# Kernel tuning notes

Hardware: AMD Instinct MI355X
Metric: run time of the kernel (lower is better)

## Reference

```python
import jax, jax.numpy as jnp
import numpy as np

DIVERSITY_RATE = 0.5


def setup_inputs() -> dict:
    key = jax.random.key(0)
    k1, k2 = jax.random.split(key)
    # model log-probabilities at current step: (bsz, beam, vocab)
    lprobs = jax.nn.log_softmax(
        jax.random.normal(k1, (128, 5, 50257), dtype=jnp.float32), axis=-1
    )
    # historical hypothesis scores: (bsz, beam, step)
    scores = jax.random.normal(k2, (128, 5, 10), dtype=jnp.float32)
    return {"lprobs": lprobs, "scores": scores, "step": 10}


def reference(lprobs, scores, step):
    bsz, beam_size, vocab_size = lprobs.shape
    k = min(beam_size * 2, beam_size * vocab_size - 1)  # = 10 here

    # step > 0 path: accumulate running score of each hypothesis
    lp = lprobs + scores[:, :, step - 1][:, :, None]  # (bsz, beam, vocab)

    # 1/ per-beam top-k over vocab (vectorized over all beams at once)
    s, idx = jax.lax.top_k(lp, k)  # (bsz, beam, k); idx already < vocab (fmod no-op)

    # 2/,3/ intra-sibling ordering -> rank penalty (rank r gets r*rate)
    sibling_score = jnp.arange(1, k + 1, dtype=lp.dtype) * DIVERSITY_RATE  # (k,)
    s = s - sibling_score  # broadcast over (bsz, beam, k)

    # 4/ final top-k over all beam*k candidates
    indices = idx.reshape(bsz, beam_size * k)
    final_scores, flat_pos = jax.lax.top_k(s.reshape(bsz, beam_size * k), k)
    final_beams = flat_pos // k  # which input beam each winner came from
    final_indices = jnp.take_along_axis(indices, flat_pos, axis=1)  # vocab ids

    return final_scores, final_indices, final_beams
```

## Files before the change

kernel.cpp:

```cpp
#include <hip/hip_runtime.h>
#include <hip/hip_bf16.h>
#include <math.h>
#include <stdint.h>


#define BS    256
#define KK    10
#define BEAM  5
#define NSLOT 7
#define CS    (BS * NSLOT * 4)
#define CAP   1024
#define FCAP  2048

typedef unsigned long long u64;

__device__ __forceinline__ uint32_t ford(float x) {
    uint32_t u = __float_as_uint(x);
    return (u & 0x80000000u) ? ~u : (u | 0x80000000u);
}
__device__ __forceinline__ float funord(uint32_t u) {
    return __uint_as_float((u & 0x80000000u) ? (u & 0x7fffffffu) : ~u);
}

__device__ __forceinline__ void insert10(u64 (&key)[KK], u64 k) {
    if (k > key[KK - 1]) {
#pragma unroll
        for (int j = KK - 1; j >= 1; --j)
            key[j] = (k > key[j - 1]) ? key[j - 1] : ((k > key[j]) ? k : key[j]);
        if (k > key[0]) key[0] = k;
    }
}

__global__ __launch_bounds__(BS) void dss_chunk_topk(
    const float* __restrict__ lprobs,
    const float* __restrict__ scores,
    const int*   __restrict__ step_ptr,
    int vocab, int sdim, int nc,
    u64* __restrict__ ws_keys)
{
    const int chunk = blockIdx.x;
    const int row   = blockIdx.y;
    const int tid   = threadIdx.x;
    const int lane  = tid & 63;
    const int step  = step_ptr[0];
    const float bias = scores[(size_t)row * sdim + (step - 1)];

    const int c0 = chunk * CS;
    int len = vocab - c0; if (len > CS) len = CS;
    const float* cp = lprobs + (size_t)row * vocab + c0;

    __shared__ u64   cand[CAP];
    __shared__ float sgrp[16];
    __shared__ int   s_cnt;

    int pre = (4 - (int)(((uintptr_t)cp >> 2) & 3)) & 3;
    if (pre > len) pre = len;
    const float4* g4 = (const float4*)(cp + pre);
    const int nvec = (len - pre) >> 2;
    const int done = pre + 4 * nvec;
    const int rem  = len - done;

    float4 v[NSLOT];
    float m = -INFINITY;
    if (nvec == NSLOT * BS) {
#pragma unroll
        for (int i = 0; i < NSLOT; ++i) v[i] = g4[tid + (i << 8)];
#pragma unroll
        for (int i = 0; i < NSLOT; ++i) {
            v[i].x += bias; v[i].y += bias; v[i].z += bias; v[i].w += bias;
            m = fmaxf(m, fmaxf(fmaxf(v[i].x, v[i].y), fmaxf(v[i].z, v[i].w)));
        }
    } else {
#pragma unroll
        for (int i = 0; i < NSLOT; ++i) {
            int idx = tid + (i << 8);
            if (idx < nvec) {
                float4 x = g4[idx];
                x.x += bias; x.y += bias; x.z += bias; x.w += bias;
                v[i] = x;
                m = fmaxf(m, fmaxf(fmaxf(x.x, x.y), fmaxf(x.z, x.w)));
            } else {
                v[i].x = -INFINITY; v[i].y = -INFINITY; v[i].z = -INFINITY; v[i].w = -INFINITY;
            }
        }
    }
    float xv = -INFINITY; int xi = -1;
    if (tid < pre)                        { xi = tid;            xv = cp[xi] + bias; }
    else if (tid >= 4 && tid < 4 + rem)   { xi = done + tid - 4; xv = cp[xi] + bias; }
    m = fmaxf(m, xv);

    if (tid == 0) s_cnt = 0;

    float gm = m;
#pragma unroll
    for (int o = 1; o <= 8; o <<= 1) gm = fmaxf(gm, __shfl_xor(gm, o));
    if ((lane & 15) == 0) sgrp[(tid >> 6) * 4 + (lane >> 4)] = gm;
    __syncthreads();
    float tau = sgrp[0];
#pragma unroll
    for (int g = 1; g < 16; ++g) tau = fminf(tau, sgrp[g]);

    auto app = [&](float x, int j) {
        if (j < len) {
            int p = atomicAdd(&s_cnt, 1);
            if (p < CAP) cand[p] = ((u64)ford(x) << 32) | (uint32_t)~(c0 + j);
        }
    };
#pragma unroll
    for (int i = 0; i < NSLOT; ++i) {
        int base = pre + ((tid + (i << 8)) << 2);
        if (v[i].x >= tau) app(v[i].x, base + 0);
        if (v[i].y >= tau) app(v[i].y, base + 1);
        if (v[i].z >= tau) app(v[i].z, base + 2);
        if (v[i].w >= tau) app(v[i].w, base + 3);
    }
    if (xi >= 0 && xv >= tau) app(xv, xi);
    __syncthreads();

    int n = s_cnt; if (n > CAP) n = CAP;
    u64* outp = ws_keys + ((size_t)row * nc + chunk) * KK;
    if (tid < KK && tid >= n) outp[tid] = 0;
    for (int t2 = tid; t2 < n; t2 += BS) {
        u64 k = cand[t2];
        int rk = 0;
        for (int j = 0; j < n; ++j) rk += (cand[j] > k) ? 1 : 0;
        if (rk < KK) outp[rk] = k;
    }
}

__global__ __launch_bounds__(512) void dss_final(
    const u64* __restrict__ ws_keys,
    float* __restrict__ out, int bsz, int nc)
{
    const int b = blockIdx.x;
    const int t = threadIdx.x;
    const int NC  = nc * KK;
    const int tot = BEAM * NC;

    __shared__ u64  kbuf[BEAM * KK * 8];
    __shared__ float pen[BEAM * KK];
    __shared__ int   pidx[BEAM * KK];

    for (int i = t; i < tot; i += 512) kbuf[i] = ws_keys[(size_t)b * tot + i];
    __syncthreads();

    if (t < tot) {
        int beam = t / NC;
        u64 k = kbuf[t];
        const u64* kb = kbuf + beam * NC;
        int r = 0;
        for (int j = 0; j < NC; ++j) r += (kb[j] > k) ? 1 : 0;
        if (r < KK) {
            pen [beam * KK + r] = funord((uint32_t)(k >> 32)) - 0.5f * (float)(r + 1);
            pidx[beam * KK + r] = (int)~(uint32_t)k;
        }
    }
    __syncthreads();

    if (t < BEAM * KK) {
        float p = pen[t];
        int r = 0;
        for (int j = 0; j < BEAM * KK; ++j) {
            float q = pen[j];
            r += (q > p || (q == p && j < t)) ? 1 : 0;
        }
        if (r < KK) {
            out[              b * KK + r] = p;
            out[(size_t)bsz * KK     + b * KK + r] = (float)pidx[t];
            out[(size_t)2 * bsz * KK + b * KK + r] = (float)(t / KK);
        }
    }
}

__global__ __launch_bounds__(BS) void dss_row_topk(
    const float* __restrict__ lprobs,
    const float* __restrict__ scores,
    const int*   __restrict__ step_ptr,
    int vocab, int sdim,
    u64* __restrict__ ws_keys)
{
    const int row = blockIdx.x;
    const int tid = threadIdx.x;
    const int step = step_ptr[0];
    const float bias = scores[(size_t)row * sdim + (step - 1)];
    const float* rp = lprobs + (size_t)row * vocab;

    __shared__ u64  cand[FCAP];
    __shared__ u64  skey[BS * KK];
    __shared__ int  cnt;
    __shared__ float sh_tau;

    int pre = (4 - (int)(((uintptr_t)rp >> 2) & 3)) & 3;
    if (pre > vocab) pre = vocab;
    const float4* p4 = (const float4*)(rp + pre);
    const int nvec = (vocab - pre) >> 2;
    const int done = pre + 4 * nvec;
    const int rem  = vocab - done;

    float m = -INFINITY;
    if (tid < pre) m = rp[tid] + bias;
    for (int t = tid; t < nvec; t += BS) {
        float4 x = p4[t];
        m = fmaxf(m, fmaxf(fmaxf(x.x + bias, x.y + bias), fmaxf(x.z + bias, x.w + bias)));
    }
    if (tid < rem) m = fmaxf(m, rp[done + tid] + bias);

    skey[tid * KK] = ((u64)ford(m) << 32) | (uint32_t)~tid;
#pragma unroll
    for (int j = 1; j < KK; ++j) skey[tid * KK + j] = 0;
    if (tid == 0) cnt = 0;
    __syncthreads();
    for (int off = BS / 2; off >= 1; off >>= 1) {
        if (tid < off) {
            const int pa = tid * KK, pb = (tid + off) * KK;
            u64 mk[KK]; int ia = 0, ib = 0;
#pragma unroll
            for (int j = 0; j < KK; ++j) {
                u64 ka = skey[pa + ia], kb = skey[pb + ib];
                bool tA = (ka >= kb); mk[j] = tA ? ka : kb;
                if (tA) ++ia; else ++ib;
            }
#pragma unroll
            for (int j = 0; j < KK; ++j) skey[pa + j] = mk[j];
        }
        __syncthreads();
    }
    if (tid == 0) sh_tau = funord((uint32_t)(skey[9] >> 32));
    __syncthreads();
    const float tau = sh_tau;

    auto app = [&](float x, int i) {
        if (x >= tau) {
            int p = atomicAdd(&cnt, 1);
            if (p < FCAP) cand[p] = ((u64)ford(x) << 32) | (uint32_t)~i;
        }
    };
    if (tid < pre) app(rp[tid] + bias, tid);
    for (int t = tid; t < nvec; t += BS) {
        float4 x = p4[t];
        int base = pre + 4 * t;
        app(x.x + bias, base + 0); app(x.y + bias, base + 1);
        app(x.z + bias, base + 2); app(x.w + bias, base + 3);
    }
    if (tid < rem) app(rp[done + tid] + bias, done + tid);
    __syncthreads();

    const int n = (cnt < FCAP) ? cnt : FCAP;
    {
        u64 key[KK];
#pragma unroll
        for (int j = 0; j < KK; ++j) key[j] = 0;
        for (int i = tid; i < n; i += BS) insert10(key, cand[i]);
#pragma unroll
        for (int j = 0; j < KK; ++j) skey[tid * KK + j] = key[j];
    }
    __syncthreads();
    for (int off = BS / 2; off >= 1; off >>= 1) {
        if (tid < off) {
            const int pa = tid * KK, pb = (tid + off) * KK;
            u64 mk[KK]; int ia = 0, ib = 0;
#pragma unroll
            for (int j = 0; j < KK; ++j) {
                u64 ka = skey[pa + ia], kb = skey[pb + ib];
                bool tA = (ka >= kb); mk[j] = tA ? ka : kb;
                if (tA) ++ia; else ++ib;
            }
#pragma unroll
            for (int j = 0; j < KK; ++j) skey[pa + j] = mk[j];
        }
        __syncthreads();
    }
    if (tid < KK) ws_keys[(size_t)row * KK + tid] = skey[tid];
}

extern "C" void kernel_launch(void* const* d_in, const int* in_sizes, int n_in,
                              void* d_out, int out_size, void* d_ws, size_t ws_size,
                              hipStream_t stream)
{
    const float* lprobs = (const float*)d_in[0];
    const float* scores = (const float*)d_in[1];
    const int*   step   = (const int*)d_in[2];

    const int bsz   = 128;
    const int rows  = bsz * BEAM;
    const int vocab = in_sizes[0] / rows;
    const int sdim  = in_sizes[1] / rows;

    u64* ws_keys = (u64*)d_ws;

    int nc = (vocab + CS - 1) / CS;
    if (nc > 8) nc = 8;
    if (ws_size < (size_t)rows * nc * KK * sizeof(u64)) nc = 1;

    if (nc > 1) {
        dss_chunk_topk<<<dim3(nc, rows), BS, 0, stream>>>(
            lprobs, scores, step, vocab, sdim, nc, ws_keys);
    } else {
        dss_row_topk<<<rows, BS, 0, stream>>>(lprobs, scores, step, vocab, sdim, ws_keys);
    }
    dss_final<<<bsz, 512, 0, stream>>>(ws_keys, (float*)d_out, bsz, nc);
}
```

Before: 197.9 us.

## Convert chunk top-k into persistent kernel with double-buffered tile prefetch

Replaces the one-block-per-chunk launch with a persistent grid of up to 1024 blocks that loop over tiles. Each block prefetches the next tile into registers while it filters and ranks the current one, and the shared candidate buffers are double-buffered. The bias add moves into key construction, and CAP drops to 512 to fit two buffers. The aim is to hide global load latency behind the selection work, at the cost of higher register pressure, which could lower occupancy or cause spills.

```diff
diff --git a/kernel.cpp b/kernel.cpp
--- a/kernel.cpp
+++ b/kernel.cpp
@@ -9,7 +9,8 @@
 #define BEAM  5
 #define NSLOT 7
 #define CS    (BS * NSLOT * 4)
-#define CAP   1024
+#define CAP   512
+#define GRID  1024
 #define FCAP  2048
 
 typedef unsigned long long u64;
@@ -31,100 +32,130 @@
     }
 }
 
-__global__ __launch_bounds__(BS) void dss_chunk_topk(
-    const float* __restrict__ lprobs,
-    const float* __restrict__ scores,
-    const int*   __restrict__ step_ptr,
-    int vocab, int sdim, int nc,
-    u64* __restrict__ ws_keys)
-{
-    const int chunk = blockIdx.x;
-    const int row   = blockIdx.y;
-    const int tid   = threadIdx.x;
-    const int lane  = tid & 63;
-    const int step  = step_ptr[0];
-    const float bias = scores[(size_t)row * sdim + (step - 1)];
-
-    const int c0 = chunk * CS;
-    int len = vocab - c0; if (len > CS) len = CS;
-    const float* cp = lprobs + (size_t)row * vocab + c0;
-
-    __shared__ u64   cand[CAP];
-    __shared__ float sgrp[16];
-    __shared__ int   s_cnt;
-
+struct Tile {
+    float4 v[NSLOT];
+    float  xv;
+    int    xi;
+    int    c0, len, pre;
+    float  bias;
+};
+
+__device__ __forceinline__ void tile_load(
+    Tile& T, int tile, int nc,
+    const float* __restrict__ lprobs, const float* __restrict__ scores,
+    int vocab, int sdim, int step, int tid)
+{
+    const int row   = tile / nc;
+    const int chunk = tile - row * nc;
+    T.bias = scores[(size_t)row * sdim + (step - 1)];
+    T.c0 = chunk * CS;
+    int len = vocab - T.c0; if (len > CS) len = CS;
+    T.len = len;
+    const float* cp = lprobs + (size_t)row * vocab + T.c0;
     int pre = (4 - (int)(((uintptr_t)cp >> 2) & 3)) & 3;
     if (pre > len) pre = len;
+    T.pre = pre;
     const float4* g4 = (const float4*)(cp + pre);
     const int nvec = (len - pre) >> 2;
     const int done = pre + 4 * nvec;
     const int rem  = len - done;
-
-    float4 v[NSLOT];
-    float m = -INFINITY;
-    if (nvec == NSLOT * BS) {
-#pragma unroll
-        for (int i = 0; i < NSLOT; ++i) v[i] = g4[tid + (i << 8)];
-#pragma unroll
-        for (int i = 0; i < NSLOT; ++i) {
-            v[i].x += bias; v[i].y += bias; v[i].z += bias; v[i].w += bias;
-            m = fmaxf(m, fmaxf(fmaxf(v[i].x, v[i].y), fmaxf(v[i].z, v[i].w)));
-        }
-    } else {
-#pragma unroll
-        for (int i = 0; i < NSLOT; ++i) {
-            int idx = tid + (i << 8);
-            if (idx < nvec) {
-                float4 x = g4[idx];
-                x.x += bias; x.y += bias; x.z += bias; x.w += bias;
-                v[i] = x;
-                m = fmaxf(m, fmaxf(fmaxf(x.x, x.y), fmaxf(x.z, x.w)));
-            } else {
-                v[i].x = -INFINITY; v[i].y = -INFINITY; v[i].z = -INFINITY; v[i].w = -INFINITY;
-            }
-        }
-    }
-    float xv = -INFINITY; int xi = -1;
-    if (tid < pre)                        { xi = tid;            xv = cp[xi] + bias; }
-    else if (tid >= 4 && tid < 4 + rem)   { xi = done + tid - 4; xv = cp[xi] + bias; }
-    m = fmaxf(m, xv);
-
-    if (tid == 0) s_cnt = 0;
+#pragma unroll
+    for (int i = 0; i < NSLOT; ++i) {
+        int idx = tid + (i << 8);
+        if (idx < nvec) T.v[i] = g4[idx];
+        else { T.v[i].x = -INFINITY; T.v[i].y = -INFINITY;
+               T.v[i].z = -INFINITY; T.v[i].w = -INFINITY; }
+    }
+    T.xv = -INFINITY; T.xi = -1;
+    if (tid < pre)                      { T.xi = tid;            T.xv = cp[T.xi]; }
+    else if (tid >= 4 && tid < 4 + rem) { T.xi = done + tid - 4; T.xv = cp[T.xi]; }
+}
+
+__device__ __forceinline__ void tile_process(
+    const Tile& T, int p, int tile, int tid, int lane,
+    u64 (*cand)[CAP], float (*sgrp)[16], int* s_cnt,
+    u64* __restrict__ ws_keys)
+{
+    float m = T.xv;
+#pragma unroll
+    for (int i = 0; i < NSLOT; ++i)
+        m = fmaxf(m, fmaxf(fmaxf(T.v[i].x, T.v[i].y), fmaxf(T.v[i].z, T.v[i].w)));
 
     float gm = m;
 #pragma unroll
     for (int o = 1; o <= 8; o <<= 1) gm = fmaxf(gm, __shfl_xor(gm, o));
-    if ((lane & 15) == 0) sgrp[(tid >> 6) * 4 + (lane >> 4)] = gm;
-    __syncthreads();
-    float tau = sgrp[0];
-#pragma unroll
-    for (int g = 1; g < 16; ++g) tau = fminf(tau, sgrp[g]);
-
+    if ((lane & 15) == 0) sgrp[p][(tid >> 6) * 4 + (lane >> 4)] = gm;
+    if (tid == 0) s_cnt[p] = 0;
+    __syncthreads();
+    float tau = sgrp[p][0];
+#pragma unroll
+    for (int g = 1; g < 16; ++g) tau = fminf(tau, sgrp[p][g]);
+
+    const float bias = T.bias;
+    const int c0 = T.c0, len = T.len, pre = T.pre;
     auto app = [&](float x, int j) {
         if (j < len) {
-            int p = atomicAdd(&s_cnt, 1);
-            if (p < CAP) cand[p] = ((u64)ford(x) << 32) | (uint32_t)~(c0 + j);
+            int pos = atomicAdd(&s_cnt[p], 1);
+            if (pos < CAP)
+                cand[p][pos] = ((u64)ford(x + bias) << 32) | (uint32_t)~(c0 + j);
         }
     };
 #pragma unroll
     for (int i = 0; i < NSLOT; ++i) {
         int base = pre + ((tid + (i << 8)) << 2);
-        if (v[i].x >= tau) app(v[i].x, base + 0);
-        if (v[i].y >= tau) app(v[i].y, base + 1);
-        if (v[i].z >= tau) app(v[i].z, base + 2);
-        if (v[i].w >= tau) app(v[i].w, base + 3);
-    }
-    if (xi >= 0 && xv >= tau) app(xv, xi);
-    __syncthreads();
-
-    int n = s_cnt; if (n > CAP) n = CAP;
-    u64* outp = ws_keys + ((size_t)row * nc + chunk) * KK;
+        if (T.v[i].x >= tau) app(T.v[i].x, base + 0);
+        if (T.v[i].y >= tau) app(T.v[i].y, base + 1);
+        if (T.v[i].z >= tau) app(T.v[i].z, base + 2);
+        if (T.v[i].w >= tau) app(T.v[i].w, base + 3);
+    }
+    if (T.xi >= 0 && T.xv >= tau) app(T.xv, T.xi);
+    __syncthreads();
+
+    int n = s_cnt[p]; if (n > CAP) n = CAP;
+    u64* outp = ws_keys + (size_t)tile * KK;
     if (tid < KK && tid >= n) outp[tid] = 0;
     for (int t2 = tid; t2 < n; t2 += BS) {
-        u64 k = cand[t2];
+        u64 k = cand[p][t2];
         int rk = 0;
-        for (int j = 0; j < n; ++j) rk += (cand[j] > k) ? 1 : 0;
+        for (int j = 0; j < n; ++j) rk += (cand[p][j] > k) ? 1 : 0;
         if (rk < KK) outp[rk] = k;
+    }
+}
+
+__global__ __launch_bounds__(BS, 4) void dss_persist(
+    const float* __restrict__ lprobs,
+    const float* __restrict__ scores,
+    const int*   __restrict__ step_ptr,
+    int vocab, int sdim, int nc, int ntiles,
+    u64* __restrict__ ws_keys)
+{
+    __shared__ u64   cand[2][CAP];
+    __shared__ float sgrp[2][16];
+    __shared__ int   s_cnt[2];
+
+    const int tid  = threadIdx.x;
+    const int lane = tid & 63;
+    const int step = step_ptr[0];
+    const int G    = gridDim.x;
+
+    int t = blockIdx.x;
+    if (t >= ntiles) return;
+
+    Tile A, B;
+    tile_load(A, t, nc, lprobs, scores, vocab, sdim, step, tid);
+    for (;;) {
+        const int tB = t + G;
+        const bool hB = tB < ntiles;
+        if (hB) tile_load(B, tB, nc, lprobs, scores, vocab, sdim, step, tid);
+        tile_process(A, 0, t, tid, lane, cand, sgrp, s_cnt, ws_keys);
+        if (!hB) break;
+
+        const int tA = tB + G;
+        const bool hA = tA < ntiles;
+        if (hA) tile_load(A, tA, nc, lprobs, scores, vocab, sdim, step, tid);
+        tile_process(B, 1, tB, tid, lane, cand, sgrp, s_cnt, ws_keys);
+        if (!hA) break;
+        t = tA;
     }
 }
 
@@ -293,8 +324,10 @@
     if (ws_size < (size_t)rows * nc * KK * sizeof(u64)) nc = 1;
 
     if (nc > 1) {
-        dss_chunk_topk<<<dim3(nc, rows), BS, 0, stream>>>(
-            lprobs, scores, step, vocab, sdim, nc, ws_keys);
+        const int ntiles = rows * nc;
+        int grid = GRID; if (grid > ntiles) grid = ntiles;
+        dss_persist<<<grid, BS, 0, stream>>>(
+            lprobs, scores, step, vocab, sdim, nc, ntiles, ws_keys);
     } else {
         dss_row_topk<<<rows, BS, 0, stream>>>(lprobs, scores, step, vocab, sdim, ws_keys);
     }
```

New measurement: 206.0 us. +4.1%, slower.
